# Kernel tuning notes

Hardware: AMD Instinct MI355X
Metric: run time of the kernel (lower is better)

The kernel has to match this reference:

```python
import jax, jax.numpy as jnp
import numpy as np

WINDOW_SIZE = 11
WINDOW_SIGMA = 1.5
LOSS_WEIGHT = 1.0
PAD = WINDOW_SIZE // 2  # 5; applied to BOTH H and W as in the torch source


def _gaussian_window(channels):
    # Matches torch gaussian_window: 1-D gaussian reshaped to (1,1,1,ws),
    # repeated per channel -> OIHW kernel of shape (C, 1, 1, ws).
    coords = np.arange(WINDOW_SIZE, dtype=np.float32) - (WINDOW_SIZE // 2)
    g = np.exp(-coords ** 2 / (2.0 * WINDOW_SIGMA ** 2))
    g = g / g.sum()
    w = np.tile(g.reshape(1, 1, 1, WINDOW_SIZE), (channels, 1, 1, 1))
    return jnp.asarray(w)


def _dwconv(x, w, channels):
    # Depthwise conv, kernel (1, ws), zero padding 5 on both H and W
    # (faithful to F.conv2d(..., padding=5) with a (1,11) kernel, which
    # grows H by 10 -- intentional reproduction of the source behavior).
    return jax.lax.conv_general_dilated(
        x, w,
        window_strides=(1, 1),
        padding=((PAD, PAD), (PAD, PAD)),
        dimension_numbers=('NCHW', 'OIHW', 'NCHW'),
        feature_group_count=channels,
    )


def setup_inputs() -> dict:
    key = jax.random.key(0)
    k1, k2 = jax.random.split(key)
    shape = (16, 3, 512, 512)
    pred = jax.random.uniform(k1, shape, dtype=jnp.float32)
    target = jax.random.uniform(k2, shape, dtype=jnp.float32)
    return {"pred": pred, "target": target}


def reference(pred, target):
    channels = pred.shape[1]
    w = _gaussian_window(channels)
    conv = lambda x: _dwconv(x, w, channels)

    mu1 = conv(pred)              # (B, C, H+10, W)
    mu2 = conv(target)
    mu1_sq = mu1 * mu1
    mu2_sq = mu2 * mu2
    mu1_mu2 = mu1 * mu2

    sigma1_sq = conv(pred * pred) - mu1_sq
    sigma2_sq = conv(target * target) - mu2_sq
    sigma12 = conv(pred * target) - mu1_mu2

    C1 = 0.01 ** 2
    C2 = 0.03 ** 2
    ssim_map = ((2.0 * mu1_mu2 + C1) * (2.0 * sigma12 + C2)) / (
        (mu1_sq + mu2_sq + C1) * (sigma1_sq + sigma2_sq + C2))

    return LOSS_WEIGHT * (1.0 - ssim_map.mean())
```

## Files before the change

kernel.cpp:

```cpp
#include <hip/hip_runtime.h>
#include <cmath>

#define WS 11

typedef float v2f __attribute__((ext_vector_type(2)));

struct GaussPairs { unsigned long long gg[WS]; };

__device__ __forceinline__ v2f pk_fma_sg(unsigned long long g, v2f b, v2f c) {
    v2f d;
    asm("v_pk_fma_f32 %0, %1, %2, %3" : "=v"(d) : "s"(g), "v"(b), "v"(c));
    return d;
}
__device__ __forceinline__ v2f pk_mul(v2f a, v2f b) {
    v2f d;
    asm("v_pk_mul_f32 %0, %1, %2" : "=v"(d) : "v"(a), "v"(b));
    return d;
}

__global__ __launch_bounds__(256) void ssim_row_kernel(
    const float* __restrict__ pred, const float* __restrict__ targ,
    GaussPairs gp, float* __restrict__ partials)
{
    const int t = threadIdx.x;
    const int lane = t & 63;
    const int wave = t >> 6;
    const int wave_id = blockIdx.x * 4 + wave;
    const float C1 = 0.0001f, C2 = 0.0009f;

    const long long off = (long long)wave_id * 512 + 8 * lane;
    const float* prow = pred + off;
    const float* trow = targ + off;

    float4 P0 = *reinterpret_cast<const float4*>(prow);
    float4 P1 = *reinterpret_cast<const float4*>(prow + 4);
    float4 Q0 = *reinterpret_cast<const float4*>(trow);
    float4 Q1 = *reinterpret_cast<const float4*>(trow + 4);

    float acc = 0.f;
    #pragma unroll
    for (int r = 0; r < 3; ++r) {
        float4 nP0, nP1, nQ0, nQ1;
        if (r < 2) {
            const float* pn = prow + (long long)(r + 1) * 8192 * 512;
            const float* tn = trow + (long long)(r + 1) * 8192 * 512;
            nP0 = *reinterpret_cast<const float4*>(pn);
            nP1 = *reinterpret_cast<const float4*>(pn + 4);
            nQ0 = *reinterpret_cast<const float4*>(tn);
            nQ1 = *reinterpret_cast<const float4*>(tn + 4);
        }

        v2f w[18], s[18];
        {
            const float pv[8] = {P0.x, P0.y, P0.z, P0.w, P1.x, P1.y, P1.z, P1.w};
            const float qv[8] = {Q0.x, Q0.y, Q0.z, Q0.w, Q1.x, Q1.y, Q1.z, Q1.w};
            #pragma unroll
            for (int i = 0; i < 8; ++i) {
                w[5 + i].x = pv[i] + qv[i];
                w[5 + i].y = pv[i] - qv[i];
            }
        }
        #pragma unroll
        for (int i = 0; i < 5; ++i) {
            float lu = __shfl_up(w[8 + i].x, 1);
            float lv = __shfl_up(w[8 + i].y, 1);
            float ru = __shfl_down(w[5 + i].x, 1);
            float rv = __shfl_down(w[5 + i].y, 1);
            w[i].x      = (lane == 0)  ? 0.f : lu;
            w[i].y      = (lane == 0)  ? 0.f : lv;
            w[13 + i].x = (lane == 63) ? 0.f : ru;
            w[13 + i].y = (lane == 63) ? 0.f : rv;
        }
        #pragma unroll
        for (int i = 0; i < 18; ++i) s[i] = pk_mul(w[i], w[i]);

        #pragma unroll
        for (int px = 0; px < 8; ++px) {
            v2f AB  = {0.f, 0.f};
            v2f SUV = {0.f, 0.f};
            #pragma unroll
            for (int k = 0; k < WS; ++k) {
                AB  = pk_fma_sg(gp.gg[k], w[px + k], AB);
                SUV = pk_fma_sg(gp.gg[k], s[px + k], SUV);
            }
            const v2f ab2 = pk_mul(AB, AB);
            const float d2 = ab2.x - ab2.y;
            const float t2 = ab2.x + ab2.y;
            const float ds = SUV.x - SUV.y;
            const float ts = SUV.x + SUV.y;
            const float num1 = fmaf(0.5f, d2, C1);
            const float den1 = fmaf(0.5f, t2, C1);
            const float num2 = fmaf(0.5f, ds - d2, C2);
            const float den2 = fmaf(0.5f, ts - t2, C2);
            acc = fmaf(num1 * num2, __builtin_amdgcn_rcpf(den1 * den2), acc);
        }

        if (r < 2) { P0 = nP0; P1 = nP1; Q0 = nQ0; Q1 = nQ1; }
    }

    #pragma unroll
    for (int offr = 32; offr > 0; offr >>= 1)
        acc += __shfl_down(acc, offr);
    __shared__ float wsum[4];
    if (lane == 0) wsum[wave] = acc;
    __syncthreads();
    if (t == 0)
        partials[blockIdx.x] = wsum[0] + wsum[1] + wsum[2] + wsum[3];
}

__global__ __launch_bounds__(256) void ssim_final_kernel(
    const float* __restrict__ partials, float* __restrict__ out)
{
    const int t = threadIdx.x;
    double d = 0.0;
    #pragma unroll
    for (int i = 0; i < 8; ++i)
        d += (double)partials[t + 256 * i];
    #pragma unroll
    for (int offr = 32; offr > 0; offr >>= 1)
        d += __shfl_down(d, offr);
    __shared__ double wsumd[4];
    const int lane = t & 63, wave = t >> 6;
    if (lane == 0) wsumd[wave] = d;
    __syncthreads();
    if (t == 0) {
        const double s = wsumd[0] + wsumd[1] + wsumd[2] + wsumd[3] + 245760.0;
        out[0] = (float)(1.0 - s / 12828672.0);
    }
}

extern "C" void kernel_launch(void* const* d_in, const int* in_sizes, int n_in,
                              void* d_out, int out_size, void* d_ws, size_t ws_size,
                              hipStream_t stream) {
    const float* pred = (const float*)d_in[0];
    const float* targ = (const float*)d_in[1];
    float* out = (float*)d_out;
    float* partials = (float*)d_ws;

    GaussPairs gp;
    double graw[WS], s = 0.0;
    for (int i = 0; i < WS; ++i) {
        const double c = (double)(i - WS / 2);
        graw[i] = exp(-c * c / (2.0 * 1.5 * 1.5));
        s += graw[i];
    }
    for (int i = 0; i < WS; ++i) {
        const float g = (float)(graw[i] / s);
        unsigned int gb;
        __builtin_memcpy(&gb, &g, 4);
        gp.gg[i] = ((unsigned long long)gb << 32) | gb;
    }

    ssim_row_kernel<<<2048, 256, 0, stream>>>(pred, targ, gp, partials);
    ssim_final_kernel<<<1, 256, 0, stream>>>(partials, out);
}
```

Baseline: 27.86 us.

## Load halo from memory, fold scale factors into weights, pack SSIM epilogue

Halo pixels are now loaded directly from global memory with clamped offsets and masked at the row edges, replacing the cross-lane shuffles. The factors 0.5 and 1/sqrt(2) are folded into two pre-scaled Gaussian weight sets so the epilogue needs no separate scaling. The scalar epilogue becomes packed v_pk_add/v_pk_mul operations that build numerator and denominator together. The cost is extra, partly redundant global loads (cache hits), dropping the explicit next-row prefetch, and small rounding changes from the pre-scaled weights.

```diff
diff --git a/kernel.cpp b/kernel.cpp
--- a/kernel.cpp
+++ b/kernel.cpp
@@ -5,7 +5,12 @@
 
 typedef float v2f __attribute__((ext_vector_type(2)));
 
-struct GaussPairs { unsigned long long gg[WS]; };
+struct GaussPairs {
+    unsigned long long gA[WS];
+    unsigned long long gS[WS];
+    unsigned long long c1c1;
+    unsigned long long c2c2;
+};
 
 __device__ __forceinline__ v2f pk_fma_sg(unsigned long long g, v2f b, v2f c) {
     v2f d;
@@ -17,6 +22,23 @@
     asm("v_pk_mul_f32 %0, %1, %2" : "=v"(d) : "v"(a), "v"(b));
     return d;
 }
+__device__ __forceinline__ v2f pk_sumdiff(v2f a) {
+    v2f d;
+    asm("v_pk_add_f32 %0, %1, %1 op_sel:[0,1] op_sel_hi:[0,1] neg_hi:[0,1]"
+        : "=v"(d) : "v"(a));
+    return d;
+}
+__device__ __forceinline__ v2f pk_add_sg(v2f a, unsigned long long c) {
+    v2f d;
+    asm("v_pk_add_f32 %0, %1, %2" : "=v"(d) : "v"(a), "s"(c));
+    return d;
+}
+__device__ __forceinline__ v2f pk_sub(v2f a, v2f b) {
+    v2f d;
+    asm("v_pk_add_f32 %0, %1, %2 neg_lo:[0,1] neg_hi:[0,1]"
+        : "=v"(d) : "v"(a), "v"(b));
+    return d;
+}
 
 __global__ __launch_bounds__(256) void ssim_row_kernel(
     const float* __restrict__ pred, const float* __restrict__ targ,
@@ -26,53 +48,56 @@
     const int lane = t & 63;
     const int wave = t >> 6;
     const int wave_id = blockIdx.x * 4 + wave;
-    const float C1 = 0.0001f, C2 = 0.0009f;
 
-    const long long off = (long long)wave_id * 512 + 8 * lane;
-    const float* prow = pred + off;
-    const float* trow = targ + off;
+    const int l8 = 8 * lane;
+    const int oL1 = (l8 - 5 < 0) ? 0 : l8 - 5;
+    const int oL4 = (l8 - 4 < 0) ? 0 : l8 - 4;
+    const int oR4 = (l8 + 8 > 504) ? 504 : l8 + 8;
+    const int oR1 = (l8 + 12 > 508) ? 508 : l8 + 12;
 
-    float4 P0 = *reinterpret_cast<const float4*>(prow);
-    float4 P1 = *reinterpret_cast<const float4*>(prow + 4);
-    float4 Q0 = *reinterpret_cast<const float4*>(trow);
-    float4 Q1 = *reinterpret_cast<const float4*>(trow + 4);
+    const float mLs = (lane == 0) ? 0.f : 1.f;
+    const float mRs = (lane == 63) ? 0.f : 1.f;
+    const v2f ML = {mLs, mLs};
+    const v2f MR = {mRs, mRs};
 
     float acc = 0.f;
     #pragma unroll
     for (int r = 0; r < 3; ++r) {
-        float4 nP0, nP1, nQ0, nQ1;
-        if (r < 2) {
-            const float* pn = prow + (long long)(r + 1) * 8192 * 512;
-            const float* tn = trow + (long long)(r + 1) * 8192 * 512;
-            nP0 = *reinterpret_cast<const float4*>(pn);
-            nP1 = *reinterpret_cast<const float4*>(pn + 4);
-            nQ0 = *reinterpret_cast<const float4*>(tn);
-            nQ1 = *reinterpret_cast<const float4*>(tn + 4);
-        }
+        const long long row = (long long)wave_id + 8192LL * r;
+        const float* prow = pred + row * 512;
+        const float* qrow = targ + row * 512;
+
+        const float  pL1 = prow[oL1];
+        const float4 pL4 = *reinterpret_cast<const float4*>(prow + oL4);
+        const float4 pA  = *reinterpret_cast<const float4*>(prow + l8);
+        const float4 pB  = *reinterpret_cast<const float4*>(prow + l8 + 4);
+        const float4 pR4 = *reinterpret_cast<const float4*>(prow + oR4);
+        const float  pR1 = prow[oR1];
+        const float  qL1 = qrow[oL1];
+        const float4 qL4 = *reinterpret_cast<const float4*>(qrow + oL4);
+        const float4 qA  = *reinterpret_cast<const float4*>(qrow + l8);
+        const float4 qB  = *reinterpret_cast<const float4*>(qrow + l8 + 4);
+        const float4 qR4 = *reinterpret_cast<const float4*>(qrow + oR4);
+        const float  qR1 = qrow[oR1];
+
+        const float pv[18] = {pL1, pL4.x, pL4.y, pL4.z, pL4.w,
+                              pA.x, pA.y, pA.z, pA.w, pB.x, pB.y, pB.z, pB.w,
+                              pR4.x, pR4.y, pR4.z, pR4.w, pR1};
+        const float qv[18] = {qL1, qL4.x, qL4.y, qL4.z, qL4.w,
+                              qA.x, qA.y, qA.z, qA.w, qB.x, qB.y, qB.z, qB.w,
+                              qR4.x, qR4.y, qR4.z, qR4.w, qR1};
 
         v2f w[18], s[18];
-        {
-            const float pv[8] = {P0.x, P0.y, P0.z, P0.w, P1.x, P1.y, P1.z, P1.w};
-            const float qv[8] = {Q0.x, Q0.y, Q0.z, Q0.w, Q1.x, Q1.y, Q1.z, Q1.w};
-            #pragma unroll
-            for (int i = 0; i < 8; ++i) {
-                w[5 + i].x = pv[i] + qv[i];
-                w[5 + i].y = pv[i] - qv[i];
-            }
+        #pragma unroll
+        for (int i = 0; i < 18; ++i) {
+            v2f wi;
+            wi.x = pv[i] + qv[i];
+            wi.y = pv[i] - qv[i];
+            if (i < 5)       wi = pk_mul(wi, ML);
+            else if (i >= 13) wi = pk_mul(wi, MR);
+            w[i] = wi;
+            s[i] = pk_mul(wi, wi);
         }
-        #pragma unroll
-        for (int i = 0; i < 5; ++i) {
-            float lu = __shfl_up(w[8 + i].x, 1);
-            float lv = __shfl_up(w[8 + i].y, 1);
-            float ru = __shfl_down(w[5 + i].x, 1);
-            float rv = __shfl_down(w[5 + i].y, 1);
-            w[i].x      = (lane == 0)  ? 0.f : lu;
-            w[i].y      = (lane == 0)  ? 0.f : lv;
-            w[13 + i].x = (lane == 63) ? 0.f : ru;
-            w[13 + i].y = (lane == 63) ? 0.f : rv;
-        }
-        #pragma unroll
-        for (int i = 0; i < 18; ++i) s[i] = pk_mul(w[i], w[i]);
 
         #pragma unroll
         for (int px = 0; px < 8; ++px) {
@@ -80,22 +105,18 @@
             v2f SUV = {0.f, 0.f};
             #pragma unroll
             for (int k = 0; k < WS; ++k) {
-                AB  = pk_fma_sg(gp.gg[k], w[px + k], AB);
-                SUV = pk_fma_sg(gp.gg[k], s[px + k], SUV);
+                AB  = pk_fma_sg(gp.gA[k], w[px + k], AB);
+                SUV = pk_fma_sg(gp.gS[k], s[px + k], SUV);
             }
-            const v2f ab2 = pk_mul(AB, AB);
-            const float d2 = ab2.x - ab2.y;
-            const float t2 = ab2.x + ab2.y;
-            const float ds = SUV.x - SUV.y;
-            const float ts = SUV.x + SUV.y;
-            const float num1 = fmaf(0.5f, d2, C1);
-            const float den1 = fmaf(0.5f, t2, C1);
-            const float num2 = fmaf(0.5f, ds - d2, C2);
-            const float den2 = fmaf(0.5f, ts - t2, C2);
-            acc = fmaf(num1 * num2, __builtin_amdgcn_rcpf(den1 * den2), acc);
+            const v2f ab2  = pk_mul(AB, AB);
+            const v2f t2d2 = pk_sumdiff(ab2);
+            const v2f tsds = pk_sumdiff(SUV);
+            const v2f dn1  = pk_add_sg(t2d2, gp.c1c1);
+            const v2f dl   = pk_sub(tsds, t2d2);
+            const v2f dn2  = pk_add_sg(dl, gp.c2c2);
+            const v2f nd   = pk_mul(dn1, dn2);
+            acc = fmaf(nd.y, __builtin_amdgcn_rcpf(nd.x), acc);
         }
-
-        if (r < 2) { P0 = nP0; P1 = nP1; Q0 = nQ0; Q1 = nQ1; }
     }
 
     #pragma unroll
@@ -129,6 +150,12 @@
     }
 }
 
+static unsigned long long pack2(float x) {
+    unsigned int b;
+    __builtin_memcpy(&b, &x, 4);
+    return ((unsigned long long)b << 32) | b;
+}
+
 extern "C" void kernel_launch(void* const* d_in, const int* in_sizes, int n_in,
                               void* d_out, int out_size, void* d_ws, size_t ws_size,
                               hipStream_t stream) {
@@ -145,11 +172,12 @@
         s += graw[i];
     }
     for (int i = 0; i < WS; ++i) {
-        const float g = (float)(graw[i] / s);
-        unsigned int gb;
-        __builtin_memcpy(&gb, &g, 4);
-        gp.gg[i] = ((unsigned long long)gb << 32) | gb;
+        const double g = graw[i] / s;
+        gp.gA[i] = pack2((float)(g * 0.70710678118654752));
+        gp.gS[i] = pack2((float)(g * 0.5));
     }
+    gp.c1c1 = pack2(0.0001f);
+    gp.c2c2 = pack2(0.0009f);
 
     ssim_row_kernel<<<2048, 256, 0, stream>>>(pred, targ, gp, partials);
     ssim_final_kernel<<<1, 256, 0, stream>>>(partials, out);
```

New measurement: 30.18 us. 1.08x slower.
